# Performance work log

Measured on AMD Instinct MI355X. Metric: run time of the kernel, lower is better.

Reference implementation:

```python
import jax, jax.numpy as jnp
import numpy as np

B, S, E, N, H = 2, 2048, 2048, 16, 128  # batch, seq, embed, heads, depth


def sine_table(features, length, min_timescale=1.0, max_timescale=10000.0):
    fraction = jnp.arange(0, features, 2, dtype=jnp.float32) / features
    timescale = min_timescale * (max_timescale / min_timescale) ** fraction
    sinusoid_inp = jnp.einsum('i,j->ij', jnp.arange(length, dtype=jnp.float32), 1.0 / timescale,
                              precision=jax.lax.Precision.HIGHEST)
    sinusoid_inp = jnp.concatenate([sinusoid_inp, sinusoid_inp], axis=-1)  # [L, features]
    return jnp.sin(sinusoid_inp), jnp.cos(sinusoid_inp)


def rotate_half(x):
    x1, x2 = jnp.split(x, 2, axis=-1)
    return jnp.concatenate([-x2, x1], axis=-1)


def apply_rotary(q, k, cos, sin):
    # q: [B,S,N,H], k: [B,T,N,H]; cos/sin: [L,H] broadcast over (seq, depth)
    qcos = cos[: q.shape[1]][None, :, None, :]
    qsin = sin[: q.shape[1]][None, :, None, :]
    kcos = cos[: k.shape[1]][None, :, None, :]
    ksin = sin[: k.shape[1]][None, :, None, :]
    return q * qcos + rotate_half(q) * qsin, k * kcos + rotate_half(k) * ksin


def setup_inputs() -> dict:
    key = jax.random.key(0)
    ks = jax.random.split(key, 6)
    scale = 1.0 / np.sqrt(E)
    return {
        'x_q': jax.random.normal(ks[0], (B, S, E), jnp.float32),
        'x_kv': jax.random.normal(ks[1], (B, S, E), jnp.float32),
        'WQ': jax.random.normal(ks[2], (E, N, H), jnp.float32) * scale,
        'WK': jax.random.normal(ks[3], (E, N, H), jnp.float32) * scale,
        'WV': jax.random.normal(ks[4], (E, N, H), jnp.float32) * scale,
        'WO': jax.random.normal(ks[5], (N, H, E), jnp.float32) * scale,
    }


def reference(x_q, x_kv, WQ, WK, WV, WO):
    q = jnp.einsum('bse,enh->bsnh', x_q, WQ)
    k = jnp.einsum('bte,enh->btnh', x_kv, WK)
    v = jnp.einsum('bte,enh->btnh', x_kv, WV)

    sin, cos = sine_table(q.shape[-1], max(q.shape[1], k.shape[1]))
    q, k = apply_rotary(q, k, cos, sin)

    # causal attention bias: [1,1,S,T]
    s_len, t_len = q.shape[1], k.shape[1]
    causal = jnp.arange(s_len)[:, None] >= jnp.arange(t_len)[None, :]
    bias = jnp.where(causal, 0.0, -1e10).astype(jnp.float32)[None, None]

    logits = jnp.einsum('bsnh,btnh->bnst', q, k) / np.sqrt(H) + bias
    probs = jax.nn.softmax(logits, axis=-1)
    a = jnp.einsum('bnst,btnh->bsnh', probs, v)
    o = jnp.einsum('bsnh,nhe->bse', a, WO)
    return o
```

## Files before the change

### kernel.cpp

```cpp
#include <hip/hip_runtime.h>
#include <hip/hip_bf16.h>

typedef __bf16 bf16;
typedef __attribute__((ext_vector_type(8))) __bf16 bf16x8;
typedef __attribute__((ext_vector_type(4))) __bf16 bf16x4;
typedef __attribute__((ext_vector_type(4))) float f32x4;

typedef const __attribute__((address_space(1))) void* gptr_t;
typedef __attribute__((address_space(3))) void* sptr_t;

__device__ __forceinline__ void gload16(const void* g, void* l) {
  __builtin_amdgcn_global_load_lds((gptr_t)g, (sptr_t)l, 16, 0, 0);
}

#define MFMA_BF16(a, b, c) __builtin_amdgcn_mfma_f32_16x16x32_bf16((a), (b), (c), 0, 0, 0)

#define BAR() do { asm volatile("" ::: "memory"); __builtin_amdgcn_s_barrier(); asm volatile("" ::: "memory"); } while (0)

namespace {
constexpr int kB = 2, kS = 2048, kE = 2048, kN = 16, kH = 128;
constexpr float kScale = 0.08838834764831845f;
constexpr float kLog2e = 1.4426950408889634f;
}

__global__ void k_cvt(const float* __restrict__ in, bf16* __restrict__ out) {
  int i = blockIdx.x * 256 + threadIdx.x;
  float4 v = reinterpret_cast<const float4*>(in)[i];
  bf16x4 o = { (bf16)v.x, (bf16)v.y, (bf16)v.z, (bf16)v.w };
  reinterpret_cast<bf16x4*>(out)[i] = o;
}

__global__ void k_tconv(const float* __restrict__ in, bf16* __restrict__ out) {
  __shared__ bf16 tile[64][66];
  int bx = blockIdx.x & 31, by = blockIdx.x >> 5;
  int r0 = by * 64, c0 = bx * 64;
  int t = threadIdx.x;
  int c = t & 63, rb = t >> 6;
#pragma unroll
  for (int j = 0; j < 16; ++j) {
    int r = rb + j * 4;
    tile[r][c] = (bf16)in[(size_t)(r0 + r) * 2048 + c0 + c];
  }
  __syncthreads();
  int rr = t & 63;
#pragma unroll
  for (int j = 0; j < 16; ++j) {
    int cc = rb + j * 4;
    out[(size_t)(c0 + cc) * 2048 + r0 + rr] = tile[rr][cc];
  }
}

__global__ void k_vtrans(const bf16* __restrict__ V, bf16* __restrict__ Vt) {
  __shared__ bf16 tile[64][66];
  int bid = blockIdx.x;
  int bn = bid >> 6;
  int s0 = ((bid >> 1) & 31) * 64;
  int h0 = (bid & 1) * 64;
  size_t base = (size_t)bn * kS * kH;
  int t = threadIdx.x, c = t & 63, rb = t >> 6;
#pragma unroll
  for (int j = 0; j < 16; ++j) {
    int r = rb + j * 4;
    tile[r][c] = V[base + (size_t)(s0 + r) * kH + h0 + c];
  }
  __syncthreads();
#pragma unroll
  for (int j = 0; j < 16; ++j) {
    int hh = rb + j * 4;
    Vt[base + (size_t)(h0 + hh) * kS + s0 + (t & 63)] = tile[t & 63][hh];
  }
}

__global__ void k_rope(bf16* __restrict__ Qd, bf16* __restrict__ Kd) {
  int tid = blockIdx.x * 256 + threadIdx.x;
  int i = tid & 63;
  int s = (tid >> 6) & (kS - 1);
  int bn = tid >> 17;
  size_t base = ((size_t)bn * kS + s) * kH;
  float inv = exp2f(-(float)i * 0.20762050593046457f);
  float ang = (float)s * inv;
  float sn, cs;
  sincosf(ang, &sn, &cs);
  float q1 = (float)Qd[base + i], q2 = (float)Qd[base + i + 64];
  Qd[base + i]      = (bf16)(q1 * cs - q2 * sn);
  Qd[base + i + 64] = (bf16)(q2 * cs + q1 * sn);
  float k1 = (float)Kd[base + i], k2 = (float)Kd[base + i + 64];
  Kd[base + i]      = (bf16)(k1 * cs - k2 * sn);
  Kd[base + i + 64] = (bf16)(k2 * cs + k1 * sn);
}


__device__ __forceinline__ void stage_half(const bf16* __restrict__ src, size_t row0,
                                           int k0, char* slot, int t) {
#pragma unroll
  for (int i = 0; i < 2; ++i) {
    int idx = i * 512 + t;
    int d = idx * 16;
    int lb = d ^ (((d >> 9) & 1) << 5);
    int r = lb >> 7;
    int kc = (lb & 127) >> 1;
    gload16(src + (row0 + r) * 2048 + k0 + kc,
            slot + i * 8192 + (t >> 6) * 1024);
  }
}

template <int MODE>
__global__ __launch_bounds__(512, 2) void k_gemm8(const bf16* __restrict__ Aq,
                                                  const bf16* __restrict__ Akv,
                                                  const bf16* __restrict__ Bt,
                                                  void* __restrict__ Cout) {
  constexpr int NTN = (MODE == 0) ? 24 : 8;
  constexpr int NT = 32;
  __shared__ __align__(16) char AsB[2][2][16384];
  __shared__ __align__(16) char BsB[2][2][16384];
  int bid = blockIdx.x;
  constexpr int nblk = 16 * NTN;
  int swz = (bid & 7) * (nblk >> 3) + (bid >> 3);
  int mt = swz / NTN, nt = swz - mt * NTN;
  size_t m0 = (size_t)mt * 256;
  int n0 = nt * 256;
  const bf16* A = (MODE == 0 && nt >= 8) ? Akv : Aq;
  int t = threadIdx.x, wid = t >> 6, lane = t & 63;
  int l16 = lane & 15, lq = lane >> 4;
  int wr = wid >> 2, wc = wid & 3;
  int bhalf = wc >> 1;
  int brow0 = ((wc & 1) << 6) + l16;

  f32x4 acc[8][4] = {};
  bf16x8 af[4], bf[4];

  stage_half(Bt, (size_t)n0,       0, BsB[0][0], t);
  stage_half(Bt, (size_t)n0 + 128, 0, BsB[0][1], t);
  stage_half(A,  m0,               0, AsB[0][0], t);
  stage_half(A,  m0 + 128,         0, AsB[0][1], t);
  stage_half(Bt, (size_t)n0,      64, BsB[1][0], t);
  stage_half(Bt, (size_t)n0 + 128, 64, BsB[1][1], t);
  asm volatile("s_waitcnt vmcnt(4)" ::: "memory");
  BAR();

  for (int kt = 0; kt < NT; ++kt) {
    int buf = kt & 1, nbuf = buf ^ 1;
#pragma unroll
    for (int j = 0; j < 4; ++j) {
      int l = ((j * 16 + l16) << 7) + (lq << 4);
      af[j] = *(const bf16x8*)(AsB[buf][wr] + (l ^ (((l >> 9) & 1) << 5)));
    }
#pragma unroll
    for (int nf = 0; nf < 4; ++nf) {
      int l = ((brow0 + nf * 16) << 7) + (lq << 4);
      bf[nf] = *(const bf16x8*)(BsB[buf][bhalf] + (l ^ (((l >> 9) & 1) << 5)));
    }
    if (kt + 1 < NT) stage_half(A, m0, (kt + 1) * 64, AsB[nbuf][0], t);
    BAR();
    __builtin_amdgcn_s_setprio(1);
#pragma unroll
    for (int j = 0; j < 4; ++j)
#pragma unroll
      for (int nf = 0; nf < 4; ++nf)
        acc[j][nf] = MFMA_BF16(af[j], bf[nf], acc[j][nf]);
    __builtin_amdgcn_s_setprio(0);
    BAR();
#pragma unroll
    for (int j = 0; j < 4; ++j) {
      int l = (((j + 4) * 16 + l16) << 7) + (lq << 4);
      af[j] = *(const bf16x8*)(AsB[buf][wr] + (l ^ (((l >> 9) & 1) << 5)));
    }
    if (kt + 1 < NT) stage_half(A, m0 + 128, (kt + 1) * 64, AsB[nbuf][1], t);
    BAR();
    __builtin_amdgcn_s_setprio(1);
#pragma unroll
    for (int j = 0; j < 4; ++j)
#pragma unroll
      for (int nf = 0; nf < 4; ++nf)
        acc[j + 4][nf] = MFMA_BF16(af[j], bf[nf], acc[j + 4][nf]);
    __builtin_amdgcn_s_setprio(0);
    BAR();
#pragma unroll
    for (int j = 0; j < 4; ++j) {
      int l = ((j * 16 + l16) << 7) + 64 + (lq << 4);
      af[j] = *(const bf16x8*)(AsB[buf][wr] + (l ^ (((l >> 9) & 1) << 5)));
    }
#pragma unroll
    for (int nf = 0; nf < 4; ++nf) {
      int l = ((brow0 + nf * 16) << 7) + 64 + (lq << 4);
      bf[nf] = *(const bf16x8*)(BsB[buf][bhalf] + (l ^ (((l >> 9) & 1) << 5)));
    }
    BAR();
    __builtin_amdgcn_s_setprio(1);
#pragma unroll
    for (int j = 0; j < 4; ++j)
#pragma unroll
      for (int nf = 0; nf < 4; ++nf)
        acc[j][nf] = MFMA_BF16(af[j], bf[nf], acc[j][nf]);
    __builtin_amdgcn_s_setprio(0);
    BAR();
#pragma unroll
    for (int j = 0; j < 4; ++j) {
      int l = (((j + 4) * 16 + l16) << 7) + 64 + (lq << 4);
      af[j] = *(const bf16x8*)(AsB[buf][wr] + (l ^ (((l >> 9) & 1) << 5)));
    }
    if (kt + 2 < NT) {
      stage_half(Bt, (size_t)n0,       (kt + 2) * 64, BsB[buf][0], t);
      stage_half(Bt, (size_t)n0 + 128, (kt + 2) * 64, BsB[buf][1], t);
    }
    BAR();
    __builtin_amdgcn_s_setprio(1);
#pragma unroll
    for (int j = 0; j < 4; ++j)
#pragma unroll
      for (int nf = 0; nf < 4; ++nf)
        acc[j + 4][nf] = MFMA_BF16(af[j], bf[nf], acc[j + 4][nf]);
    __builtin_amdgcn_s_setprio(0);
    if (kt < NT - 2)       asm volatile("s_waitcnt vmcnt(4)" ::: "memory");
    else if (kt == NT - 2) asm volatile("s_waitcnt vmcnt(0)" ::: "memory");
    BAR();
  }

#pragma unroll
  for (int mf = 0; mf < 8; ++mf) {
    int rowb = (int)m0 + wr * 128 + mf * 16 + lq * 4;
#pragma unroll
    for (int nf = 0; nf < 4; ++nf) {
      int col = n0 + wc * 64 + nf * 16 + l16;
#pragma unroll
      for (int r = 0; r < 4; ++r) {
        float v = acc[mf][nf][r];
        int mrow = rowb + r;
        if (MODE == 0) {
          int grp = col >> 11, cw = col & 2047;
          int b = mrow >> 11, s = mrow & 2047, n = cw >> 7, h = cw & 127;
          ((bf16*)Cout)[(size_t)grp * 8388608 +
                        (((size_t)(b * 16 + n) * 2048 + s) << 7) + h] = (bf16)v;
        } else {
          ((float*)Cout)[((size_t)mrow << 11) + col] = v;
        }
      }
    }
  }
}

__global__ __launch_bounds__(512, 4) void k_attn(const bf16* __restrict__ Q,
                                                 const bf16* __restrict__ Kg,
                                                 const bf16* __restrict__ Vt,
                                                 bf16* __restrict__ AO) {
  __shared__ __align__(16) bf16 Ks[64 * 128];
  __shared__ __align__(16) bf16 Vs[128 * 64];
  __shared__ __align__(16) bf16 Ps[8][16][72];
  int bid = blockIdx.x;
  int half = bid >> 8;
  int bn = (half << 4) | ((bid >> 4) & 15);
  int qt = (bid & 15) ^ (half ? 15 : 0);
  int q0 = qt * 128;
  int t = threadIdx.x, wid = t >> 6, lane = t & 63;
  int l16 = lane & 15, lq = lane >> 4;
  size_t bnSH = (size_t)bn * kS * kH;

  int qrow_a = q0 + wid * 16 + l16;
  bf16x8 qf[4];
#pragma unroll
  for (int ks = 0; ks < 4; ++ks)
    qf[ks] = *(const bf16x8*)(Q + bnSH + (size_t)qrow_a * kH + ks * 32 + lq * 8);

  f32x4 oacc[8] = {};
  float mrun[4], lrun[4];
#pragma unroll
  for (int r = 0; r < 4; ++r) { mrun[r] = -1e30f; lrun[r] = 0.f; }

  int ntiles = (q0 + 128) >> 6;
  for (int kt = 0; kt < ntiles; ++kt) {
    int kv0 = kt * 64;
#pragma unroll
    for (int i = 0; i < 2; ++i) {
      int idx = i * 512 + t;
      {
        int row = idx >> 4, ch = idx & 15;
        int gch = ch ^ (row & 7);
        gload16(Kg + bnSH + (size_t)(kv0 + row) * kH + gch * 8,
                (char*)Ks + i * 8192 + wid * 1024);
      }
      {
        int row = idx >> 3, ch = idx & 7;
        int gch = ch ^ (row & 7);
        gload16(Vt + bnSH + (size_t)row * kS + kv0 + gch * 8,
                (char*)Vs + i * 8192 + wid * 1024);
      }
    }
    __syncthreads();

    f32x4 sacc[4] = {};
#pragma unroll
    for (int ks = 0; ks < 4; ++ks) {
#pragma unroll
      for (int ni = 0; ni < 4; ++ni) {
        int sp = ni * 16 + l16;
        int hb = (ks * 32 + lq * 8) * 2;
        bf16x8 kb = *(const bf16x8*)((const char*)Ks + sp * 256 + (hb ^ ((sp & 7) << 4)));
        sacc[ni] = MFMA_BF16(qf[ks], kb, sacc[ni]);
      }
    }

    bool need_mask = (kv0 + 63) > (q0 + wid * 16);
#pragma unroll
    for (int ni = 0; ni < 4; ++ni) {
      f32x4 v = sacc[ni] * kScale;
      if (need_mask) {
#pragma unroll
        for (int r = 0; r < 4; ++r) {
          int qrow = q0 + wid * 16 + lq * 4 + r;
          int col = kv0 + ni * 16 + l16;
          if (col > qrow) v[r] = -1e30f;
        }
      }
      sacc[ni] = v;
    }

#pragma unroll
    for (int r = 0; r < 4; ++r) {
      float pm = fmaxf(fmaxf(sacc[0][r], sacc[1][r]),
                       fmaxf(sacc[2][r], sacc[3][r]));
      pm = fmaxf(pm, __shfl_xor(pm, 1));
      pm = fmaxf(pm, __shfl_xor(pm, 2));
      pm = fmaxf(pm, __shfl_xor(pm, 4));
      pm = fmaxf(pm, __shfl_xor(pm, 8));
      float mold = mrun[r];
      float mnew = fmaxf(mold, pm);
      float alpha = exp2f((mold - mnew) * kLog2e);
      mrun[r] = mnew;
      float rs = 0.f;
#pragma unroll
      for (int ni = 0; ni < 4; ++ni) {
        float p = exp2f((sacc[ni][r] - mnew) * kLog2e);
        sacc[ni][r] = p;
        rs += p;
      }
      rs += __shfl_xor(rs, 1);
      rs += __shfl_xor(rs, 2);
      rs += __shfl_xor(rs, 4);
      rs += __shfl_xor(rs, 8);
      lrun[r] = lrun[r] * alpha + rs;
#pragma unroll
      for (int nj = 0; nj < 8; ++nj) oacc[nj][r] *= alpha;
    }

#pragma unroll
    for (int ni = 0; ni < 4; ++ni)
#pragma unroll
      for (int r = 0; r < 4; ++r)
        Ps[wid][lq * 4 + r][ni * 16 + l16] = (bf16)sacc[ni][r];

#pragma unroll
    for (int ks = 0; ks < 2; ++ks) {
      bf16x8 pa = *(const bf16x8*)&Ps[wid][l16][ks * 32 + lq * 8];
#pragma unroll
      for (int nj = 0; nj < 8; ++nj) {
        int h = nj * 16 + l16;
        int sb = (ks * 64 + lq * 16) ^ ((h & 7) << 4);
        bf16x8 vb = *(const bf16x8*)((const char*)Vs + h * 128 + sb);
        oacc[nj] = MFMA_BF16(pa, vb, oacc[nj]);
      }
    }
    __syncthreads();
  }

  int b = bn >> 4, n = bn & 15;
#pragma unroll
  for (int r = 0; r < 4; ++r) {
    float inv = 1.0f / lrun[r];
    int qrow = q0 + wid * 16 + lq * 4 + r;
#pragma unroll
    for (int nj = 0; nj < 8; ++nj) {
      float v = oacc[nj][r] * inv;
      AO[(((size_t)b * kS + qrow) * kN + n) * kH + nj * 16 + l16] = (bf16)v;
    }
  }
}

extern "C" void kernel_launch(void* const* d_in, const int* in_sizes, int n_in,
                              void* d_out, int out_size, void* d_ws, size_t ws_size,
                              hipStream_t stream) {
  (void)in_sizes; (void)n_in; (void)out_size; (void)ws_size;
  const float* x_q  = (const float*)d_in[0];
  const float* x_kv = (const float*)d_in[1];
  const float* WQ   = (const float*)d_in[2];
  const float* WK   = (const float*)d_in[3];
  const float* WV   = (const float*)d_in[4];
  const float* WO   = (const float*)d_in[5];
  float* out = (float*)d_out;
  char* w = (char*)d_ws;
  const size_t MB = 1ull << 20;
  bf16* xq  = (bf16*)(w + 0 * MB);
  bf16* xkv = (bf16*)(w + 16 * MB);
  bf16* WqT = (bf16*)(w + 32 * MB);
  bf16* WkT = (bf16*)(w + 40 * MB);
  bf16* WvT = (bf16*)(w + 48 * MB);
  bf16* WoT = (bf16*)(w + 56 * MB);
  bf16* Qb  = (bf16*)(w + 64 * MB);
  bf16* Kb  = (bf16*)(w + 80 * MB);
  bf16* Vb  = (bf16*)(w + 96 * MB);
  bf16* AO  = xq;
  bf16* Vtb = xkv;

  k_cvt<<<8192, 256, 0, stream>>>(x_q, xq);
  k_cvt<<<8192, 256, 0, stream>>>(x_kv, xkv);
  k_tconv<<<1024, 256, 0, stream>>>(WQ, WqT);
  k_tconv<<<1024, 256, 0, stream>>>(WK, WkT);
  k_tconv<<<1024, 256, 0, stream>>>(WV, WvT);
  k_tconv<<<1024, 256, 0, stream>>>(WO, WoT);
  k_gemm8<0><<<384, 512, 0, stream>>>(xq, xkv, WqT, Qb);
  k_rope<<<16384, 256, 0, stream>>>(Qb, Kb);
  k_vtrans<<<2048, 256, 0, stream>>>(Vb, Vtb);
  k_attn<<<512, 512, 0, stream>>>(Qb, Kb, Vtb, AO);
  k_gemm8<1><<<128, 512, 0, stream>>>(AO, AO, WoT, out);
}
```

Before: 474.6 us.

## Retile output GEMM to 128-row tiles, widen LDS swizzle, precompute RoPE tables

The output-projection GEMM now uses 128-row M tiles with a triple-buffered B ring, doubling its grid from 128 to 256 blocks so more CUs have work. The LDS XOR swizzle is changed from a single-bit pattern to a 3-bit row-based pattern, aimed at cutting bank conflicts on fragment reads. RoPE sin/cos values are computed once into a table by a new kernel instead of per element for every batch and head. The trade-offs are an extra launch and table reads in the RoPE path, and less B reuse per block in the output GEMM.

```diff
diff --git a/kernel.cpp b/kernel.cpp
--- a/kernel.cpp
+++ b/kernel.cpp
@@ -16,6 +16,8 @@
 #define MFMA_BF16(a, b, c) __builtin_amdgcn_mfma_f32_16x16x32_bf16((a), (b), (c), 0, 0, 0)
 
 #define BAR() do { asm volatile("" ::: "memory"); __builtin_amdgcn_s_barrier(); asm volatile("" ::: "memory"); } while (0)
+
+__device__ __forceinline__ int swzb(int l) { return l ^ (((l >> 7) & 7) << 4); }
 
 namespace {
 constexpr int kB = 2, kS = 2048, kE = 2048, kN = 16, kH = 128;
@@ -71,16 +73,25 @@
   }
 }
 
-__global__ void k_rope(bf16* __restrict__ Qd, bf16* __restrict__ Kd) {
+__global__ void k_trig(float* __restrict__ ctab, float* __restrict__ stab) {
+  int tid = blockIdx.x * 256 + threadIdx.x;
+  int s = tid >> 6, i = tid & 63;
+  float inv = exp2f(-(float)i * 0.20762050593046457f);
+  float ang = (float)s * inv;
+  float sn, cs;
+  sincosf(ang, &sn, &cs);
+  ctab[tid] = cs;
+  stab[tid] = sn;
+}
+
+__global__ void k_rope(bf16* __restrict__ Qd, bf16* __restrict__ Kd,
+                       const float* __restrict__ ctab, const float* __restrict__ stab) {
   int tid = blockIdx.x * 256 + threadIdx.x;
   int i = tid & 63;
   int s = (tid >> 6) & (kS - 1);
   int bn = tid >> 17;
   size_t base = ((size_t)bn * kS + s) * kH;
-  float inv = exp2f(-(float)i * 0.20762050593046457f);
-  float ang = (float)s * inv;
-  float sn, cs;
-  sincosf(ang, &sn, &cs);
+  float cs = ctab[(s << 6) + i], sn = stab[(s << 6) + i];
   float q1 = (float)Qd[base + i], q2 = (float)Qd[base + i + 64];
   Qd[base + i]      = (bf16)(q1 * cs - q2 * sn);
   Qd[base + i + 64] = (bf16)(q2 * cs + q1 * sn);
@@ -96,13 +107,18 @@
   for (int i = 0; i < 2; ++i) {
     int idx = i * 512 + t;
     int d = idx * 16;
-    int lb = d ^ (((d >> 9) & 1) << 5);
+    int lb = d ^ (((d >> 7) & 7) << 4);
     int r = lb >> 7;
     int kc = (lb & 127) >> 1;
     gload16(src + (row0 + r) * 2048 + k0 + kc,
             slot + i * 8192 + (t >> 6) * 1024);
   }
 }
+
+#define ASB(b, h) ((char*)LDS + (b) * 32768 + (h) * 16384)
+#define BSB(b, h) ((char*)LDS + 65536 + (b) * 32768 + (h) * 16384)
+#define AS1(b)    ((char*)LDS + (b) * 16384)
+#define BS1(q, h) ((char*)LDS + 32768 + (q) * 32768 + (h) * 16384)
 
 template <int MODE>
 __global__ __launch_bounds__(512, 2) void k_gemm8(const bf16* __restrict__ Aq,
@@ -110,14 +126,15 @@
                                                   const bf16* __restrict__ Bt,
                                                   void* __restrict__ Cout) {
   constexpr int NTN = (MODE == 0) ? 24 : 8;
+  constexpr int NTM = (MODE == 0) ? 16 : 32;
   constexpr int NT = 32;
-  __shared__ __align__(16) char AsB[2][2][16384];
-  __shared__ __align__(16) char BsB[2][2][16384];
+  constexpr int BM = (MODE == 0) ? 256 : 128;
+  __shared__ __align__(16) char LDS[131072];
   int bid = blockIdx.x;
-  constexpr int nblk = 16 * NTN;
+  constexpr int nblk = NTM * NTN;
   int swz = (bid & 7) * (nblk >> 3) + (bid >> 3);
   int mt = swz / NTN, nt = swz - mt * NTN;
-  size_t m0 = (size_t)mt * 256;
+  size_t m0 = (size_t)mt * BM;
   int n0 = nt * 256;
   const bf16* A = (MODE == 0 && nt >= 8) ? Akv : Aq;
   int t = threadIdx.x, wid = t >> 6, lane = t & 63;
@@ -126,99 +143,193 @@
   int bhalf = wc >> 1;
   int brow0 = ((wc & 1) << 6) + l16;
 
-  f32x4 acc[8][4] = {};
-  bf16x8 af[4], bf[4];
-
-  stage_half(Bt, (size_t)n0,       0, BsB[0][0], t);
-  stage_half(Bt, (size_t)n0 + 128, 0, BsB[0][1], t);
-  stage_half(A,  m0,               0, AsB[0][0], t);
-  stage_half(A,  m0 + 128,         0, AsB[0][1], t);
-  stage_half(Bt, (size_t)n0,      64, BsB[1][0], t);
-  stage_half(Bt, (size_t)n0 + 128, 64, BsB[1][1], t);
-  asm volatile("s_waitcnt vmcnt(4)" ::: "memory");
-  BAR();
-
-  for (int kt = 0; kt < NT; ++kt) {
-    int buf = kt & 1, nbuf = buf ^ 1;
-#pragma unroll
-    for (int j = 0; j < 4; ++j) {
-      int l = ((j * 16 + l16) << 7) + (lq << 4);
-      af[j] = *(const bf16x8*)(AsB[buf][wr] + (l ^ (((l >> 9) & 1) << 5)));
-    }
-#pragma unroll
-    for (int nf = 0; nf < 4; ++nf) {
-      int l = ((brow0 + nf * 16) << 7) + (lq << 4);
-      bf[nf] = *(const bf16x8*)(BsB[buf][bhalf] + (l ^ (((l >> 9) & 1) << 5)));
-    }
-    if (kt + 1 < NT) stage_half(A, m0, (kt + 1) * 64, AsB[nbuf][0], t);
+  constexpr int MF = (MODE == 0) ? 8 : 4;
+  f32x4 acc[MF][4] = {};
+  bf16x8 af[4], bfr[4];
+
+  if constexpr (MODE == 0) {
+    stage_half(Bt, (size_t)n0,       0, BSB(0, 0), t);
+    stage_half(Bt, (size_t)n0 + 128, 0, BSB(0, 1), t);
+    stage_half(A,  m0,               0, ASB(0, 0), t);
+    stage_half(A,  m0 + 128,         0, ASB(0, 1), t);
+    stage_half(Bt, (size_t)n0,      64, BSB(1, 0), t);
+    stage_half(Bt, (size_t)n0 + 128, 64, BSB(1, 1), t);
+    asm volatile("s_waitcnt vmcnt(4)" ::: "memory");
     BAR();
-    __builtin_amdgcn_s_setprio(1);
-#pragma unroll
-    for (int j = 0; j < 4; ++j)
-#pragma unroll
-      for (int nf = 0; nf < 4; ++nf)
-        acc[j][nf] = MFMA_BF16(af[j], bf[nf], acc[j][nf]);
-    __builtin_amdgcn_s_setprio(0);
+
+    for (int kt = 0; kt < NT; ++kt) {
+      int buf = kt & 1, nbuf = buf ^ 1;
+#pragma unroll
+      for (int j = 0; j < 4; ++j) {
+        int l = ((j * 16 + l16) << 7) + (lq << 4);
+        af[j] = *(const bf16x8*)(ASB(buf, wr) + swzb(l));
+      }
+#pragma unroll
+      for (int nf = 0; nf < 4; ++nf) {
+        int l = ((brow0 + nf * 16) << 7) + (lq << 4);
+        bfr[nf] = *(const bf16x8*)(BSB(buf, bhalf) + swzb(l));
+      }
+      if (kt + 1 < NT) stage_half(A, m0, (kt + 1) * 64, ASB(nbuf, 0), t);
+      BAR();
+      __builtin_amdgcn_s_setprio(1);
+#pragma unroll
+      for (int j = 0; j < 4; ++j)
+#pragma unroll
+        for (int nf = 0; nf < 4; ++nf)
+          acc[j][nf] = MFMA_BF16(af[j], bfr[nf], acc[j][nf]);
+      __builtin_amdgcn_s_setprio(0);
+      BAR();
+#pragma unroll
+      for (int j = 0; j < 4; ++j) {
+        int l = (((j + 4) * 16 + l16) << 7) + (lq << 4);
+        af[j] = *(const bf16x8*)(ASB(buf, wr) + swzb(l));
+      }
+      if (kt + 1 < NT) stage_half(A, m0 + 128, (kt + 1) * 64, ASB(nbuf, 1), t);
+      BAR();
+      __builtin_amdgcn_s_setprio(1);
+#pragma unroll
+      for (int j = 0; j < 4; ++j)
+#pragma unroll
+        for (int nf = 0; nf < 4; ++nf)
+          acc[j + 4][nf] = MFMA_BF16(af[j], bfr[nf], acc[j + 4][nf]);
+      __builtin_amdgcn_s_setprio(0);
+      BAR();
+#pragma unroll
+      for (int j = 0; j < 4; ++j) {
+        int l = ((j * 16 + l16) << 7) + 64 + (lq << 4);
+        af[j] = *(const bf16x8*)(ASB(buf, wr) + swzb(l));
+      }
+#pragma unroll
+      for (int nf = 0; nf < 4; ++nf) {
+        int l = ((brow0 + nf * 16) << 7) + 64 + (lq << 4);
+        bfr[nf] = *(const bf16x8*)(BSB(buf, bhalf) + swzb(l));
+      }
+      BAR();
+      __builtin_amdgcn_s_setprio(1);
+#pragma unroll
+      for (int j = 0; j < 4; ++j)
+#pragma unroll
+        for (int nf = 0; nf < 4; ++nf)
+          acc[j][nf] = MFMA_BF16(af[j], bfr[nf], acc[j][nf]);
+      __builtin_amdgcn_s_setprio(0);
+      BAR();
+#pragma unroll
+      for (int j = 0; j < 4; ++j) {
+        int l = (((j + 4) * 16 + l16) << 7) + 64 + (lq << 4);
+        af[j] = *(const bf16x8*)(ASB(buf, wr) + swzb(l));
+      }
+      if (kt + 2 < NT) {
+        stage_half(Bt, (size_t)n0,       (kt + 2) * 64, BSB(buf, 0), t);
+        stage_half(Bt, (size_t)n0 + 128, (kt + 2) * 64, BSB(buf, 1), t);
+      }
+      BAR();
+      __builtin_amdgcn_s_setprio(1);
+#pragma unroll
+      for (int j = 0; j < 4; ++j)
+#pragma unroll
+        for (int nf = 0; nf < 4; ++nf)
+          acc[j + 4][nf] = MFMA_BF16(af[j], bfr[nf], acc[j + 4][nf]);
+      __builtin_amdgcn_s_setprio(0);
+      if (kt < NT - 2)       asm volatile("s_waitcnt vmcnt(4)" ::: "memory");
+      else if (kt == NT - 2) asm volatile("s_waitcnt vmcnt(0)" ::: "memory");
+      BAR();
+    }
+  } else {
+    stage_half(Bt, (size_t)n0,       0, BS1(0, 0), t);
+    stage_half(Bt, (size_t)n0 + 128, 0, BS1(0, 1), t);
+    stage_half(A,  m0,               0, AS1(0), t);
+    stage_half(Bt, (size_t)n0,      64, BS1(1, 0), t);
+    stage_half(Bt, (size_t)n0 + 128, 64, BS1(1, 1), t);
+    asm volatile("s_waitcnt vmcnt(4)" ::: "memory");
     BAR();
-#pragma unroll
-    for (int j = 0; j < 4; ++j) {
-      int l = (((j + 4) * 16 + l16) << 7) + (lq << 4);
-      af[j] = *(const bf16x8*)(AsB[buf][wr] + (l ^ (((l >> 9) & 1) << 5)));
-    }
-    if (kt + 1 < NT) stage_half(A, m0 + 128, (kt + 1) * 64, AsB[nbuf][1], t);
-    BAR();
-    __builtin_amdgcn_s_setprio(1);
-#pragma unroll
-    for (int j = 0; j < 4; ++j)
-#pragma unroll
-      for (int nf = 0; nf < 4; ++nf)
-        acc[j + 4][nf] = MFMA_BF16(af[j], bf[nf], acc[j + 4][nf]);
-    __builtin_amdgcn_s_setprio(0);
-    BAR();
-#pragma unroll
-    for (int j = 0; j < 4; ++j) {
-      int l = ((j * 16 + l16) << 7) + 64 + (lq << 4);
-      af[j] = *(const bf16x8*)(AsB[buf][wr] + (l ^ (((l >> 9) & 1) << 5)));
-    }
-#pragma unroll
-    for (int nf = 0; nf < 4; ++nf) {
-      int l = ((brow0 + nf * 16) << 7) + 64 + (lq << 4);
-      bf[nf] = *(const bf16x8*)(BsB[buf][bhalf] + (l ^ (((l >> 9) & 1) << 5)));
-    }
-    BAR();
-    __builtin_amdgcn_s_setprio(1);
-#pragma unroll
-    for (int j = 0; j < 4; ++j)
-#pragma unroll
-      for (int nf = 0; nf < 4; ++nf)
-        acc[j][nf] = MFMA_BF16(af[j], bf[nf], acc[j][nf]);
-    __builtin_amdgcn_s_setprio(0);
-    BAR();
-#pragma unroll
-    for (int j = 0; j < 4; ++j) {
-      int l = (((j + 4) * 16 + l16) << 7) + 64 + (lq << 4);
-      af[j] = *(const bf16x8*)(AsB[buf][wr] + (l ^ (((l >> 9) & 1) << 5)));
-    }
-    if (kt + 2 < NT) {
-      stage_half(Bt, (size_t)n0,       (kt + 2) * 64, BsB[buf][0], t);
-      stage_half(Bt, (size_t)n0 + 128, (kt + 2) * 64, BsB[buf][1], t);
-    }
-    BAR();
-    __builtin_amdgcn_s_setprio(1);
-#pragma unroll
-    for (int j = 0; j < 4; ++j)
-#pragma unroll
-      for (int nf = 0; nf < 4; ++nf)
-        acc[j + 4][nf] = MFMA_BF16(af[j], bf[nf], acc[j + 4][nf]);
-    __builtin_amdgcn_s_setprio(0);
-    if (kt < NT - 2)       asm volatile("s_waitcnt vmcnt(4)" ::: "memory");
-    else if (kt == NT - 2) asm volatile("s_waitcnt vmcnt(0)" ::: "memory");
-    BAR();
-  }
-
-#pragma unroll
-  for (int mf = 0; mf < 8; ++mf) {
-    int rowb = (int)m0 + wr * 128 + mf * 16 + lq * 4;
+
+    int bql = 0;
+    for (int kt = 0; kt < NT; ++kt) {
+      char* Ab = AS1(kt & 1);
+      char* Anb = AS1((kt & 1) ^ 1);
+      char* Bb = BS1(bql, bhalf);
+      int bq2 = bql + 2; if (bq2 >= 3) bq2 -= 3;
+#pragma unroll
+      for (int j = 0; j < 4; ++j) {
+        int l = (((wr * 4 + j) * 16 + l16) << 7) + (lq << 4);
+        af[j] = *(const bf16x8*)(Ab + swzb(l));
+      }
+#pragma unroll
+      for (int nf = 0; nf < 2; ++nf) {
+        int l = ((brow0 + nf * 16) << 7) + (lq << 4);
+        bfr[nf] = *(const bf16x8*)(Bb + swzb(l));
+      }
+      if (kt + 1 < NT) stage_half(A, m0, (kt + 1) * 64, Anb, t);
+      BAR();
+      __builtin_amdgcn_s_setprio(1);
+#pragma unroll
+      for (int j = 0; j < 4; ++j)
+#pragma unroll
+        for (int nf = 0; nf < 2; ++nf)
+          acc[j][nf] = MFMA_BF16(af[j], bfr[nf], acc[j][nf]);
+      __builtin_amdgcn_s_setprio(0);
+      BAR();
+#pragma unroll
+      for (int nf = 0; nf < 2; ++nf) {
+        int l = ((brow0 + (nf + 2) * 16) << 7) + (lq << 4);
+        bfr[2 + nf] = *(const bf16x8*)(Bb + swzb(l));
+      }
+      if (kt + 2 < NT) {
+        stage_half(Bt, (size_t)n0,       (kt + 2) * 64, BS1(bq2, 0), t);
+        stage_half(Bt, (size_t)n0 + 128, (kt + 2) * 64, BS1(bq2, 1), t);
+      }
+      BAR();
+      __builtin_amdgcn_s_setprio(1);
+#pragma unroll
+      for (int j = 0; j < 4; ++j)
+#pragma unroll
+        for (int nf = 0; nf < 2; ++nf)
+          acc[j][2 + nf] = MFMA_BF16(af[j], bfr[2 + nf], acc[j][2 + nf]);
+      __builtin_amdgcn_s_setprio(0);
+      BAR();
+#pragma unroll
+      for (int j = 0; j < 4; ++j) {
+        int l = (((wr * 4 + j) * 16 + l16) << 7) + 64 + (lq << 4);
+        af[j] = *(const bf16x8*)(Ab + swzb(l));
+      }
+#pragma unroll
+      for (int nf = 0; nf < 2; ++nf) {
+        int l = ((brow0 + nf * 16) << 7) + 64 + (lq << 4);
+        bfr[nf] = *(const bf16x8*)(Bb + swzb(l));
+      }
+      BAR();
+      __builtin_amdgcn_s_setprio(1);
+#pragma unroll
+      for (int j = 0; j < 4; ++j)
+#pragma unroll
+        for (int nf = 0; nf < 2; ++nf)
+          acc[j][nf] = MFMA_BF16(af[j], bfr[nf], acc[j][nf]);
+      __builtin_amdgcn_s_setprio(0);
+      BAR();
+#pragma unroll
+      for (int nf = 0; nf < 2; ++nf) {
+        int l = ((brow0 + (nf + 2) * 16) << 7) + 64 + (lq << 4);
+        bfr[2 + nf] = *(const bf16x8*)(Bb + swzb(l));
+      }
+      BAR();
+      __builtin_amdgcn_s_setprio(1);
+#pragma unroll
+      for (int j = 0; j < 4; ++j)
+#pragma unroll
+        for (int nf = 0; nf < 2; ++nf)
+          acc[j][2 + nf] = MFMA_BF16(af[j], bfr[2 + nf], acc[j][2 + nf]);
+      __builtin_amdgcn_s_setprio(0);
+      if (kt < NT - 2)       asm volatile("s_waitcnt vmcnt(4)" ::: "memory");
+      else if (kt == NT - 2) asm volatile("s_waitcnt vmcnt(0)" ::: "memory");
+      BAR();
+      bql += 1; if (bql >= 3) bql -= 3;
+    }
+  }
+
+  constexpr int WRS = (MODE == 0) ? 128 : 64;
+#pragma unroll
+  for (int mf = 0; mf < MF; ++mf) {
+    int rowb = (int)m0 + wr * WRS + mf * 16 + lq * 4;
 #pragma unroll
     for (int nf = 0; nf < 4; ++nf) {
       int col = n0 + wc * 64 + nf * 16 + l16;
@@ -397,6 +508,8 @@
   bf16* Qb  = (bf16*)(w + 64 * MB);
   bf16* Kb  = (bf16*)(w + 80 * MB);
   bf16* Vb  = (bf16*)(w + 96 * MB);
+  float* ctab = (float*)(w + 0 * MB);
+  float* stab = (float*)(w + 1 * MB);
   bf16* AO  = xq;
   bf16* Vtb = xkv;
 
@@ -407,8 +520,9 @@
   k_tconv<<<1024, 256, 0, stream>>>(WV, WvT);
   k_tconv<<<1024, 256, 0, stream>>>(WO, WoT);
   k_gemm8<0><<<384, 512, 0, stream>>>(xq, xkv, WqT, Qb);
-  k_rope<<<16384, 256, 0, stream>>>(Qb, Kb);
+  k_trig<<<512, 256, 0, stream>>>(ctab, stab);
+  k_rope<<<16384, 256, 0, stream>>>(Qb, Kb, ctab, stab);
   k_vtrans<<<2048, 256, 0, stream>>>(Vb, Vtb);
   k_attn<<<512, 512, 0, stream>>>(Qb, Kb, Vtb, AO);
-  k_gemm8<1><<<128, 512, 0, stream>>>(AO, AO, WoT, out);
-}
+  k_gemm8<1><<<256, 512, 0, stream>>>(AO, AO, WoT, out);
+}
```

Measured after the change: 447.6 us. 5.7% less time.
